# Kernel tuning notes

Measured on AMD Instinct MI355X. Metric: run time of the kernel, lower is better.

## Reference

```python
import jax, jax.numpy as jnp
import numpy as np


def _mlp(x, w1, b1, w2, b2):
    # generic 2-layer MLP (stand-in for ConfiguredModule's combine_mlp / embedding_mlp)
    return jax.nn.gelu(x @ w1 + b1) @ w2 + b2


def setup_inputs() -> dict:
    key = jax.random.key(0)
    ks = jax.random.split(key, 8)
    B, N, A = 8, 128, 64          # molecules, atoms, nfeature
    Rr, Ra = 32, 16               # radial / angular geometry shifts
    P = N * (N - 1) // 2          # 8128 atom pairs
    d_pair, H, nembed = 32, 512, 256

    def rnd(k, shp, scale=1.0):
        return jax.random.normal(k, shp, dtype=jnp.float32) * scale

    return {
        "gr": rnd(ks[0], (B, N, Rr, N), 0.1),
        "ga": rnd(ks[1], (B, N, Ra, P), 0.1),
        "afv": rnd(ks[2], (B, N, A)),
        # combine_mlp: 2A -> 2A -> d_pair
        "cw1": rnd(ks[3], (2 * A, 2 * A), 1.0 / np.sqrt(2 * A)),
        "cb1": jnp.zeros((2 * A,), jnp.float32),
        "cw2": rnd(ks[4], (2 * A, d_pair), 1.0 / np.sqrt(2 * A)),
        "cb2": jnp.zeros((d_pair,), jnp.float32),
        # embedding_mlp: Rr*A + Ra*d_pair -> H -> nembed
        "ew1": rnd(ks[5], (Rr * A + Ra * d_pair, H), 1.0 / np.sqrt(Rr * A + Ra * d_pair)),
        "eb1": jnp.zeros((H,), jnp.float32),
        "ew2": rnd(ks[6], (H, nembed), 1.0 / np.sqrt(H)),
        "eb2": jnp.zeros((nembed,), jnp.float32),
    }


def reference(gr, ga, afv, cw1, cb1, cw2, cb2, ew1, eb1, ew2, eb2):
    B, N, A = afv.shape
    # _combine_afv_1: pairwise outer sum/product, upper-triangular (i<j) pairs.
    # Instead of materializing [B, 2A, N, N] and masking, gather pairs directly
    # (row-major i<j order matches torch's triu boolean-mask indexing).
    ii, jj = jnp.triu_indices(N, k=1)           # [P]
    ai = afv[:, ii, :]                           # [B, P, A]
    aj = afv[:, jj, :]                           # [B, P, A]
    afv_pair = jnp.concatenate([ai + aj, ai * aj], axis=-1)  # [B, P, 2A]
    afv_pair = _mlp(afv_pair, cw1, cb1, cw2, cb2)            # [B, P, d_pair]

    # grv = matmul(gr, afv[:, None]) : [B, N, Rr, N] @ [B, 1, N, A] -> [B, N, Rr, A]
    grv = jnp.einsum('bnrm,bma->bnra', gr, afv).reshape(B, N, -1)
    # gav = matmul(ga, afv_pair[:, None]) : [B, N, Ra, P] @ [B, 1, P, d] -> [B, N, Ra, d]
    gav = jnp.einsum('bnap,bpd->bnad', ga, afv_pair).reshape(B, N, -1)

    aef = _mlp(jnp.concatenate([grv, gav], axis=-1), ew1, eb1, ew2, eb2)  # [B, N, nembed]
    return aef, afv
```

## Files before the change

kernel.cpp:

```cpp
#include <hip/hip_runtime.h>
#include <math.h>

#define BB 8
#define NN 128
#define AA 64
#define RR 32
#define RA 16
#define PP 8128
#define DP 32
#define HH 512
#define EE 256
#define XDIM 2560

static constexpr size_t WS_PAIRT = 0;
static constexpr size_t WS_XB    = WS_PAIRT + (size_t)BB*DP*PP/2;
static constexpr size_t WS_EW1B  = WS_XB + (size_t)BB*NN*XDIM/2;
static constexpr size_t WS_AFVT  = WS_EW1B + (size_t)HH*XDIM/2;
static constexpr size_t WS_CW1T  = WS_AFVT + (size_t)BB*AA*NN/2;
static constexpr size_t WS_CW2T  = WS_CW1T + (size_t)128*128/2;
static constexpr size_t WS_EW2B  = WS_CW2T + (size_t)DP*128/2;
static constexpr size_t WS_HB    = WS_EW2B + (size_t)EE*HH/2;

typedef __attribute__((ext_vector_type(8))) short bf16x8;
typedef __attribute__((ext_vector_type(4))) float f32x4;

__device__ __forceinline__ float gelu_f(float x) {
    float u = 0.7978845608028654f * (x + 0.044715f * x * x * x);
    float au = fabsf(u);
    float e = __expf(-2.0f * au);
    float th = (1.0f - e) / (1.0f + e);
    th = copysignf(th, u);
    return 0.5f * x * (1.0f + th);
}

__device__ __forceinline__ unsigned short f2bf(float x) {
    union { float f; unsigned u; } v; v.f = x;
    unsigned r = v.u + 0x7fffu + ((v.u >> 16) & 1u);
    return (unsigned short)(r >> 16);
}

__device__ __forceinline__ bf16x8 pack_bf16x8(float4 a, float4 b) {
    bf16x8 r;
    r[0] = (short)f2bf(a.x); r[1] = (short)f2bf(a.y);
    r[2] = (short)f2bf(a.z); r[3] = (short)f2bf(a.w);
    r[4] = (short)f2bf(b.x); r[5] = (short)f2bf(b.y);
    r[6] = (short)f2bf(b.z); r[7] = (short)f2bf(b.w);
    return r;
}

__global__ __launch_bounds__(256) void prep_k(
    const float* __restrict__ afv, const float* __restrict__ cw1,
    const float* __restrict__ cw2, unsigned short* __restrict__ afvT,
    unsigned short* __restrict__ cw1T, unsigned short* __restrict__ cw2T,
    float* __restrict__ out2)
{
    const int bid = blockIdx.x, t = threadIdx.x;
    if (bid < 64) {
        int idx = bid * 256 + t;
        int b = idx >> 11;
        int rem = idx & 2047;
        int a = rem >> 5;
        int m0 = (rem & 31) * 4;
        ushort4 o;
        o.x = f2bf(afv[((size_t)b * NN + m0 + 0) * AA + a]);
        o.y = f2bf(afv[((size_t)b * NN + m0 + 1) * AA + a]);
        o.z = f2bf(afv[((size_t)b * NN + m0 + 2) * AA + a]);
        o.w = f2bf(afv[((size_t)b * NN + m0 + 3) * AA + a]);
        *(ushort4*)(afvT + ((size_t)b * AA + a) * NN + m0) = o;
        float4 v = *(const float4*)(afv + (size_t)idx * 4);
        *(float4*)(out2 + (size_t)idx * 4) = v;
    } else if (bid < 80) {
        int idx = (bid - 64) * 256 + t;
        int n = idx >> 5;
        int k0 = (idx & 31) * 4;
        ushort4 o;
        o.x = f2bf(cw1[(size_t)(k0 + 0) * 128 + n]);
        o.y = f2bf(cw1[(size_t)(k0 + 1) * 128 + n]);
        o.z = f2bf(cw1[(size_t)(k0 + 2) * 128 + n]);
        o.w = f2bf(cw1[(size_t)(k0 + 3) * 128 + n]);
        *(ushort4*)(cw1T + (size_t)n * 128 + k0) = o;
    } else {
        int idx = (bid - 80) * 256 + t;
        int d = idx >> 5;
        int k0 = (idx & 31) * 4;
        ushort4 o;
        o.x = f2bf(cw2[(size_t)(k0 + 0) * DP + d]);
        o.y = f2bf(cw2[(size_t)(k0 + 1) * DP + d]);
        o.z = f2bf(cw2[(size_t)(k0 + 2) * DP + d]);
        o.w = f2bf(cw2[(size_t)(k0 + 3) * DP + d]);
        *(ushort4*)(cw2T + (size_t)d * 128 + k0) = o;
    }
}

#define NB_GRV 256
#define NB_PAIR 1016
#define NB_EW1 1280

__global__ __launch_bounds__(256) void stage1_k(
    const float* __restrict__ afv, const unsigned short* __restrict__ cw1T,
    const float* __restrict__ cb1, const unsigned short* __restrict__ cw2T,
    const float* __restrict__ cb2, unsigned short* __restrict__ pairT,
    const float* __restrict__ gr, unsigned short* __restrict__ Xb,
    const unsigned short* __restrict__ afvT,
    const float* __restrict__ ew1, unsigned short* __restrict__ ew1bT,
    const float* __restrict__ ew2, unsigned short* __restrict__ ew2bT)
{
    __shared__ unsigned short sm[16384];
    __shared__ int iis[64], jjs[64];
    const int bid = blockIdx.x;
    const int t = threadIdx.x;
    const int w = t >> 6, lane = t & 63;
    const int lm = lane & 15, lg = lane >> 4;

    if (bid >= NB_GRV + NB_PAIR + NB_EW1) {
        int q = (bid - (NB_GRV + NB_PAIR + NB_EW1)) * 256 + t;
        int n = q & 255;
        int k0 = (q >> 8) * 4;
        ushort4 o;
        o.x = f2bf(ew2[(size_t)(k0 + 0) * EE + n]);
        o.y = f2bf(ew2[(size_t)(k0 + 1) * EE + n]);
        o.z = f2bf(ew2[(size_t)(k0 + 2) * EE + n]);
        o.w = f2bf(ew2[(size_t)(k0 + 3) * EE + n]);
        *(ushort4*)(ew2bT + (size_t)n * HH + k0) = o;
        return;
    }
    if (bid >= NB_GRV + NB_PAIR) {
        int q = (bid - (NB_GRV + NB_PAIR)) * 256 + t;
        int n = q & 511;
        int k0 = (q >> 9) * 4;
        ushort4 o;
        o.x = f2bf(ew1[(size_t)(k0 + 0) * HH + n]);
        o.y = f2bf(ew1[(size_t)(k0 + 1) * HH + n]);
        o.z = f2bf(ew1[(size_t)(k0 + 2) * HH + n]);
        o.w = f2bf(ew1[(size_t)(k0 + 3) * HH + n]);
        *(ushort4*)(ew1bT + (size_t)n * XDIM + k0) = o;
        return;
    }

    if (bid < NB_GRV) {
        const int b = bid >> 5;
        const int rbase = (bid & 31) * 128;
        const float* gab = gr + ((size_t)b * 4096 + rbase) * NN;
        unsigned short* As = sm;
        const int srow = t >> 1, half = t & 1;
        const float* arow = gab + (size_t)srow * NN + half * 64;
        #pragma unroll
        for (int q = 0; q < 8; ++q) {
            float4 x0 = *(const float4*)(arow + q * 8);
            float4 x1 = *(const float4*)(arow + q * 8 + 4);
            bf16x8 v = pack_bf16x8(x0, x1);
            int g = half * 8 + q;
            *(bf16x8*)(As + srow * 128 + ((g ^ (srow & 7)) * 8)) = v;
        }
        __syncthreads();
        const int wm = w * 32;
        f32x4 acc[2][4];
        #pragma unroll
        for (int i = 0; i < 2; ++i)
            #pragma unroll
            for (int j = 0; j < 4; ++j) acc[i][j] = 0.f;
        const unsigned short* Bb = afvT + (size_t)b * AA * NN;
        #pragma unroll
        for (int ks = 0; ks < 4; ++ks) {
            int g = ks * 4 + lg;
            int r0 = wm + lm, r1 = wm + 16 + lm;
            bf16x8 a0 = *(const bf16x8*)(As + r0 * 128 + ((g ^ (r0 & 7)) * 8));
            bf16x8 a1 = *(const bf16x8*)(As + r1 * 128 + ((g ^ (r1 & 7)) * 8));
            #pragma unroll
            for (int ni = 0; ni < 4; ++ni) {
                bf16x8 bv = *(const bf16x8*)(Bb + (size_t)(ni * 16 + lm) * NN + ks * 32 + lg * 8);
                acc[0][ni] = __builtin_amdgcn_mfma_f32_16x16x32_bf16(a0, bv, acc[0][ni], 0, 0, 0);
                acc[1][ni] = __builtin_amdgcn_mfma_f32_16x16x32_bf16(a1, bv, acc[1][ni], 0, 0, 0);
            }
        }
        __syncthreads();
        unsigned short* T = sm;
        #pragma unroll
        for (int mi = 0; mi < 2; ++mi)
            #pragma unroll
            for (int ni = 0; ni < 4; ++ni)
                #pragma unroll
                for (int r = 0; r < 4; ++r)
                    T[(wm + mi * 16 + lg * 4 + r) * 64 + ni * 16 + lm] =
                        f2bf(acc[mi][ni][r]);
        __syncthreads();
        #pragma unroll
        for (int q = 0; q < 4; ++q) {
            int idx = t + q * 256;
            int rr2 = idx >> 3, slot = idx & 7;
            bf16x8 v = *(const bf16x8*)(T + rr2 * 64 + slot * 8);
            int grow = rbase + rr2;
            *(bf16x8*)(Xb + ((size_t)(b * NN) + (grow >> 5)) * XDIM +
                       (grow & 31) * 64 + slot * 8) = v;
        }
        return;
    }

    const int bid2 = bid - NB_GRV;
    const int b = bid2 / 127;
    const int pbase = (bid2 % 127) * 64;
    unsigned short* X = sm;
    unsigned short* Hs = sm + 8192;

    if (t < 64) {
        int p = pbase + t;
        int i = 0;
        while (i < 126) {
            int nx = i + 1;
            int off = nx * 127 - (nx * (nx - 1)) / 2;
            if (off <= p) i = nx; else break;
        }
        int off = i * 127 - (i * (i - 1)) / 2;
        iis[t] = i;
        jjs[t] = i + 1 + (p - off);
    }
    __syncthreads();
    {
        int pp = t & 63, seg = t >> 6;
        const float* ar = afv + (size_t)(b * NN + iis[pp]) * AA + seg * 16;
        const float* br = afv + (size_t)(b * NN + jjs[pp]) * AA + seg * 16;
        float4 xa = *(const float4*)(ar),     xb2 = *(const float4*)(ar + 4);
        float4 xc = *(const float4*)(ar + 8), xd = *(const float4*)(ar + 12);
        float4 ya = *(const float4*)(br),     yb = *(const float4*)(br + 4);
        float4 yc = *(const float4*)(br + 8), yd = *(const float4*)(br + 12);
        float4 s0 = make_float4(xa.x + ya.x, xa.y + ya.y, xa.z + ya.z, xa.w + ya.w);
        float4 s1 = make_float4(xb2.x + yb.x, xb2.y + yb.y, xb2.z + yb.z, xb2.w + yb.w);
        float4 s2 = make_float4(xc.x + yc.x, xc.y + yc.y, xc.z + yc.z, xc.w + yc.w);
        float4 s3 = make_float4(xd.x + yd.x, xd.y + yd.y, xd.z + yd.z, xd.w + yd.w);
        float4 p0 = make_float4(xa.x * ya.x, xa.y * ya.y, xa.z * ya.z, xa.w * ya.w);
        float4 p1 = make_float4(xb2.x * yb.x, xb2.y * yb.y, xb2.z * yb.z, xb2.w * yb.w);
        float4 p2 = make_float4(xc.x * yc.x, xc.y * yc.y, xc.z * yc.z, xc.w * yc.w);
        float4 p3 = make_float4(xd.x * yd.x, xd.y * yd.y, xd.z * yd.z, xd.w * yd.w);
        int gs = seg * 2, gp = 8 + seg * 2, sw = pp & 7;
        *(bf16x8*)(X + pp * 128 + (((gs + 0) ^ sw) * 8)) = pack_bf16x8(s0, s1);
        *(bf16x8*)(X + pp * 128 + (((gs + 1) ^ sw) * 8)) = pack_bf16x8(s2, s3);
        *(bf16x8*)(X + pp * 128 + (((gp + 0) ^ sw) * 8)) = pack_bf16x8(p0, p1);
        *(bf16x8*)(X + pp * 128 + (((gp + 1) ^ sw) * 8)) = pack_bf16x8(p2, p3);
    }
    __syncthreads();
    const int wn = w * 32;
    f32x4 acc1[4][2];
    #pragma unroll
    for (int i = 0; i < 4; ++i)
        #pragma unroll
        for (int j = 0; j < 2; ++j) acc1[i][j] = 0.f;
    #pragma unroll
    for (int ks = 0; ks < 4; ++ks) {
        int g = ks * 4 + lg;
        bf16x8 a[4];
        #pragma unroll
        for (int mi = 0; mi < 4; ++mi) {
            int row = mi * 16 + lm;
            a[mi] = *(const bf16x8*)(X + row * 128 + ((g ^ (row & 7)) * 8));
        }
        #pragma unroll
        for (int ni = 0; ni < 2; ++ni) {
            bf16x8 bv = *(const bf16x8*)(cw1T + (size_t)(wn + ni * 16 + lm) * 128 +
                                         ks * 32 + lg * 8);
            #pragma unroll
            for (int mi = 0; mi < 4; ++mi)
                acc1[mi][ni] = __builtin_amdgcn_mfma_f32_16x16x32_bf16(
                    a[mi], bv, acc1[mi][ni], 0, 0, 0);
        }
    }
    #pragma unroll
    for (int ni = 0; ni < 2; ++ni) {
        int n = wn + ni * 16 + lm;
        float bb = cb1[n];
        int gn = n >> 3, ne = n & 7;
        #pragma unroll
        for (int mi = 0; mi < 4; ++mi)
            #pragma unroll
            for (int r = 0; r < 4; ++r) {
                int row = mi * 16 + lg * 4 + r;
                Hs[row * 128 + ((gn ^ (row & 7)) * 8 + ne)] =
                    f2bf(gelu_f(acc1[mi][ni][r] + bb));
            }
    }
    __syncthreads();
    f32x4 acc2[2];
    acc2[0] = 0.f; acc2[1] = 0.f;
    #pragma unroll
    for (int ks = 0; ks < 4; ++ks) {
        int row = w * 16 + lm;
        int g = ks * 4 + lg;
        bf16x8 a2 = *(const bf16x8*)(Hs + row * 128 + ((g ^ (row & 7)) * 8));
        #pragma unroll
        for (int ni = 0; ni < 2; ++ni) {
            bf16x8 bv = *(const bf16x8*)(cw2T + (size_t)(ni * 16 + lm) * 128 +
                                         ks * 32 + lg * 8);
            acc2[ni] = __builtin_amdgcn_mfma_f32_16x16x32_bf16(a2, bv, acc2[ni], 0, 0, 0);
        }
    }
    {
        unsigned short* T = sm;
        #pragma unroll
        for (int ni = 0; ni < 2; ++ni) {
            int d = ni * 16 + lm;
            float bb = cb2[d];
            #pragma unroll
            for (int r = 0; r < 4; ++r) {
                int p = w * 16 + lg * 4 + r;
                T[d * 64 + p] = f2bf(acc2[ni][r] + bb);
            }
        }
        __syncthreads();
        int d = t >> 3, slot = t & 7;
        bf16x8 v = *(const bf16x8*)(T + d * 64 + slot * 8);
        *(bf16x8*)(pairT + ((size_t)b * DP + d) * PP + pbase + slot * 8) = v;
    }
}

__global__ __launch_bounds__(256) void gav_k(
    const float* __restrict__ ga, const unsigned short* __restrict__ pairT,
    unsigned short* __restrict__ Xb)
{
    __shared__ unsigned short As[32 * 64];
    __shared__ unsigned short Bs[32 * 64];
    const int bid = blockIdx.x;
    const int rt = bid & 63, b = bid >> 6;
    const int rbase = rt * 32;
    const int t = threadIdx.x;
    const int srow = t >> 3, slot = t & 7;
    const int w = t >> 6, lane = t & 63;
    const int lm = lane & 15, lg = lane >> 4;
    const int wr = (w & 1) * 16, wc = (w >> 1) * 16;

    f32x4 acc = 0.f;

    const float* gab = ga + (size_t)(b * 2048 + rbase) * PP;
    const unsigned short* pbT = pairT + (size_t)b * DP * PP;

    float4 ra0, ra1;
    bf16x8 rb;
    ra0 = *(const float4*)(gab + (size_t)srow * PP + slot * 8);
    ra1 = *(const float4*)(gab + (size_t)srow * PP + slot * 8 + 4);
    rb  = *(const bf16x8*)(pbT + (size_t)srow * PP + slot * 8);

    for (int it = 0; it < 127; ++it) {
        __syncthreads();
        int g = (slot ^ (srow & 7)) * 8;
        *(bf16x8*)(As + srow * 64 + g) = pack_bf16x8(ra0, ra1);
        *(bf16x8*)(Bs + srow * 64 + g) = rb;
        __syncthreads();
        if (it + 1 < 127) {
            int kn = (it + 1) * 64;
            ra0 = *(const float4*)(gab + (size_t)srow * PP + kn + slot * 8);
            ra1 = *(const float4*)(gab + (size_t)srow * PP + kn + slot * 8 + 4);
            rb  = *(const bf16x8*)(pbT + (size_t)srow * PP + kn + slot * 8);
        }
        #pragma unroll
        for (int ks = 0; ks < 2; ++ks) {
            int gg = ks * 4 + lg;
            int rowa = wr + lm;
            int rowb = wc + lm;
            bf16x8 a  = *(const bf16x8*)(As + rowa * 64 + ((gg ^ (rowa & 7)) * 8));
            bf16x8 bv = *(const bf16x8*)(Bs + rowb * 64 + ((gg ^ (rowb & 7)) * 8));
            acc = __builtin_amdgcn_mfma_f32_16x16x32_bf16(a, bv, acc, 0, 0, 0);
        }
    }
    #pragma unroll
    for (int r = 0; r < 4; ++r) {
        int grow = rbase + wr + lg * 4 + r;
        int n = grow >> 4, a2 = grow & 15;
        int d = wc + lm;
        Xb[(size_t)(b * NN + n) * XDIM + 2048 + a2 * DP + d] = f2bf(acc[r]);
    }
}

__global__ __launch_bounds__(256) void mlp1_k(
    const unsigned short* __restrict__ Xb,
    const unsigned short* __restrict__ Wt,
    const float* __restrict__ eb1, unsigned short* __restrict__ Hb)
{
    __shared__ unsigned short As[64 * 64];
    __shared__ unsigned short Bs[64 * 64];
    const int bid = blockIdx.x;
    const int ct = bid & 7, rt = bid >> 3;
    const int rbase = rt * 64, nbase = ct * 64;
    const int t = threadIdx.x;
    const int w = t >> 6, lane = t & 63;
    const int lm = lane & 15, lg = lane >> 4;
    const int srow = t >> 2, sg = (t & 3) * 2;

    f32x4 acc[4];
    #pragma unroll
    for (int i = 0; i < 4; ++i) acc[i] = 0.f;

    const unsigned short* Arow = Xb + (size_t)(rbase + srow) * XDIM;
    const unsigned short* Brow = Wt + (size_t)(nbase + srow) * XDIM;

    bf16x8 rA0, rA1, rB0, rB1;
    rA0 = *(const bf16x8*)(Arow + sg * 8);
    rA1 = *(const bf16x8*)(Arow + sg * 8 + 8);
    rB0 = *(const bf16x8*)(Brow + sg * 8);
    rB1 = *(const bf16x8*)(Brow + sg * 8 + 8);

    for (int it = 0; it < 40; ++it) {
        __syncthreads();
        int sw = srow & 7;
        *(bf16x8*)(As + srow * 64 + (((sg + 0) ^ sw) * 8)) = rA0;
        *(bf16x8*)(As + srow * 64 + (((sg + 1) ^ sw) * 8)) = rA1;
        *(bf16x8*)(Bs + srow * 64 + (((sg + 0) ^ sw) * 8)) = rB0;
        *(bf16x8*)(Bs + srow * 64 + (((sg + 1) ^ sw) * 8)) = rB1;
        __syncthreads();
        if (it + 1 < 40) {
            int kn = (it + 1) * 64;
            rA0 = *(const bf16x8*)(Arow + kn + sg * 8);
            rA1 = *(const bf16x8*)(Arow + kn + sg * 8 + 8);
            rB0 = *(const bf16x8*)(Brow + kn + sg * 8);
            rB1 = *(const bf16x8*)(Brow + kn + sg * 8 + 8);
        }
        #pragma unroll
        for (int ks = 0; ks < 2; ++ks) {
            int rowa = w * 16 + lm;
            int g = ks * 4 + lg;
            bf16x8 a = *(const bf16x8*)(As + rowa * 64 + ((g ^ (rowa & 7)) * 8));
            #pragma unroll
            for (int ni = 0; ni < 4; ++ni) {
                int rowb = ni * 16 + lm;
                bf16x8 bv = *(const bf16x8*)(Bs + rowb * 64 + ((g ^ (rowb & 7)) * 8));
                acc[ni] = __builtin_amdgcn_mfma_f32_16x16x32_bf16(a, bv, acc[ni], 0, 0, 0);
            }
        }
    }
    #pragma unroll
    for (int ni = 0; ni < 4; ++ni) {
        int col = nbase + ni * 16 + lm;
        float bb = eb1[col];
        #pragma unroll
        for (int r = 0; r < 4; ++r) {
            int row = rbase + w * 16 + lg * 4 + r;
            Hb[(size_t)row * HH + col] = f2bf(gelu_f(acc[ni][r] + bb));
        }
    }
}

__global__ __launch_bounds__(256) void mlp2_k(
    const unsigned short* __restrict__ Hb,
    const unsigned short* __restrict__ Wt,
    const float* __restrict__ eb2, float* __restrict__ out)
{
    __shared__ unsigned short As[64 * 64];
    __shared__ unsigned short Bs[64 * 64];
    const int bid = blockIdx.x;
    const int ct = bid & 3, rt = bid >> 2;
    const int rbase = rt * 64, nbase = ct * 64;
    const int t = threadIdx.x;
    const int w = t >> 6, lane = t & 63;
    const int lm = lane & 15, lg = lane >> 4;
    const int srow = t >> 2, sg = (t & 3) * 2;

    f32x4 acc[4];
    #pragma unroll
    for (int i = 0; i < 4; ++i) acc[i] = 0.f;

    const unsigned short* Arow = Hb + (size_t)(rbase + srow) * HH;
    const unsigned short* Brow = Wt + (size_t)(nbase + srow) * HH;

    bf16x8 rA0, rA1, rB0, rB1;
    rA0 = *(const bf16x8*)(Arow + sg * 8);
    rA1 = *(const bf16x8*)(Arow + sg * 8 + 8);
    rB0 = *(const bf16x8*)(Brow + sg * 8);
    rB1 = *(const bf16x8*)(Brow + sg * 8 + 8);

    for (int it = 0; it < 8; ++it) {
        __syncthreads();
        int sw = srow & 7;
        *(bf16x8*)(As + srow * 64 + (((sg + 0) ^ sw) * 8)) = rA0;
        *(bf16x8*)(As + srow * 64 + (((sg + 1) ^ sw) * 8)) = rA1;
        *(bf16x8*)(Bs + srow * 64 + (((sg + 0) ^ sw) * 8)) = rB0;
        *(bf16x8*)(Bs + srow * 64 + (((sg + 1) ^ sw) * 8)) = rB1;
        __syncthreads();
        if (it + 1 < 8) {
            int kn = (it + 1) * 64;
            rA0 = *(const bf16x8*)(Arow + kn + sg * 8);
            rA1 = *(const bf16x8*)(Arow + kn + sg * 8 + 8);
            rB0 = *(const bf16x8*)(Brow + kn + sg * 8);
            rB1 = *(const bf16x8*)(Brow + kn + sg * 8 + 8);
        }
        #pragma unroll
        for (int ks = 0; ks < 2; ++ks) {
            int rowa = w * 16 + lm;
            int g = ks * 4 + lg;
            bf16x8 a = *(const bf16x8*)(As + rowa * 64 + ((g ^ (rowa & 7)) * 8));
            #pragma unroll
            for (int ni = 0; ni < 4; ++ni) {
                int rowb = ni * 16 + lm;
                bf16x8 bv = *(const bf16x8*)(Bs + rowb * 64 + ((g ^ (rowb & 7)) * 8));
                acc[ni] = __builtin_amdgcn_mfma_f32_16x16x32_bf16(a, bv, acc[ni], 0, 0, 0);
            }
        }
    }
    #pragma unroll
    for (int ni = 0; ni < 4; ++ni) {
        int col = nbase + ni * 16 + lm;
        float bb = eb2[col];
        #pragma unroll
        for (int r = 0; r < 4; ++r) {
            int row = rbase + w * 16 + lg * 4 + r;
            out[(size_t)row * EE + col] = acc[ni][r] + bb;
        }
    }
}

extern "C" void kernel_launch(void* const* d_in, const int* in_sizes, int n_in,
                              void* d_out, int out_size, void* d_ws, size_t ws_size,
                              hipStream_t stream) {
    const float* gr  = (const float*)d_in[0];
    const float* ga  = (const float*)d_in[1];
    const float* afv = (const float*)d_in[2];
    const float* cw1 = (const float*)d_in[3];
    const float* cb1 = (const float*)d_in[4];
    const float* cw2 = (const float*)d_in[5];
    const float* cb2 = (const float*)d_in[6];
    const float* ew1 = (const float*)d_in[7];
    const float* eb1 = (const float*)d_in[8];
    const float* ew2 = (const float*)d_in[9];
    const float* eb2 = (const float*)d_in[10];
    float* out = (float*)d_out;
    float* ws = (float*)d_ws;

    unsigned short* pairT  = (unsigned short*)(ws + WS_PAIRT);
    unsigned short* Xb     = (unsigned short*)(ws + WS_XB);
    unsigned short* ew1bT  = (unsigned short*)(ws + WS_EW1B);
    unsigned short* afvT   = (unsigned short*)(ws + WS_AFVT);
    unsigned short* cw1T   = (unsigned short*)(ws + WS_CW1T);
    unsigned short* cw2T   = (unsigned short*)(ws + WS_CW2T);
    unsigned short* ew2bT  = (unsigned short*)(ws + WS_EW2B);
    unsigned short* Hb     = (unsigned short*)(ws + WS_HB);

    prep_k<<<dim3(84), dim3(256), 0, stream>>>(afv, cw1, cw2, afvT, cw1T, cw2T,
                                               out + (size_t)BB * NN * EE);
    stage1_k<<<dim3(2680), dim3(256), 0, stream>>>(afv, cw1T, cb1, cw2T, cb2, pairT,
                                                   gr, Xb, afvT, ew1, ew1bT,
                                                   ew2, ew2bT);
    gav_k<<<dim3(512), dim3(256), 0, stream>>>(ga, pairT, Xb);
    mlp1_k<<<dim3(128), dim3(256), 0, stream>>>(Xb, ew1bT, eb1, Hb);
    mlp2_k<<<dim3(64), dim3(256), 0, stream>>>(Hb, ew2bT, eb2, out);
}
```

Measured before the change: 201.3 us.

## Move weight conversion into gav kernel, double gav K-tile, halve MLP row tiles

The ew1/ew2 bf16 transpose blocks move from stage1 into the gav kernel launch, so they run alongside the memory-bound ga GEMM instead of lengthening stage1. The gav kernel now stages 128-wide K tiles, halving the loop trip count and barrier count, with a clamped tail load and a shortened final iteration. The MLP kernels use 32-row tiles so twice as many blocks launch and more CUs are filled. In exchange, each block gets less reuse and does more redundant loads of the weight tiles.

```diff
diff --git a/kernel.cpp b/kernel.cpp
--- a/kernel.cpp
+++ b/kernel.cpp
@@ -94,16 +94,13 @@
 
 #define NB_GRV 256
 #define NB_PAIR 1016
-#define NB_EW1 1280
 
 __global__ __launch_bounds__(256) void stage1_k(
     const float* __restrict__ afv, const unsigned short* __restrict__ cw1T,
     const float* __restrict__ cb1, const unsigned short* __restrict__ cw2T,
     const float* __restrict__ cb2, unsigned short* __restrict__ pairT,
     const float* __restrict__ gr, unsigned short* __restrict__ Xb,
-    const unsigned short* __restrict__ afvT,
-    const float* __restrict__ ew1, unsigned short* __restrict__ ew1bT,
-    const float* __restrict__ ew2, unsigned short* __restrict__ ew2bT)
+    const unsigned short* __restrict__ afvT)
 {
     __shared__ unsigned short sm[16384];
     __shared__ int iis[64], jjs[64];
@@ -111,31 +108,6 @@
     const int t = threadIdx.x;
     const int w = t >> 6, lane = t & 63;
     const int lm = lane & 15, lg = lane >> 4;
-
-    if (bid >= NB_GRV + NB_PAIR + NB_EW1) {
-        int q = (bid - (NB_GRV + NB_PAIR + NB_EW1)) * 256 + t;
-        int n = q & 255;
-        int k0 = (q >> 8) * 4;
-        ushort4 o;
-        o.x = f2bf(ew2[(size_t)(k0 + 0) * EE + n]);
-        o.y = f2bf(ew2[(size_t)(k0 + 1) * EE + n]);
-        o.z = f2bf(ew2[(size_t)(k0 + 2) * EE + n]);
-        o.w = f2bf(ew2[(size_t)(k0 + 3) * EE + n]);
-        *(ushort4*)(ew2bT + (size_t)n * HH + k0) = o;
-        return;
-    }
-    if (bid >= NB_GRV + NB_PAIR) {
-        int q = (bid - (NB_GRV + NB_PAIR)) * 256 + t;
-        int n = q & 511;
-        int k0 = (q >> 9) * 4;
-        ushort4 o;
-        o.x = f2bf(ew1[(size_t)(k0 + 0) * HH + n]);
-        o.y = f2bf(ew1[(size_t)(k0 + 1) * HH + n]);
-        o.z = f2bf(ew1[(size_t)(k0 + 2) * HH + n]);
-        o.w = f2bf(ew1[(size_t)(k0 + 3) * HH + n]);
-        *(ushort4*)(ew1bT + (size_t)n * XDIM + k0) = o;
-        return;
-    }
 
     if (bid < NB_GRV) {
         const int b = bid >> 5;
@@ -313,14 +285,42 @@
 
 __global__ __launch_bounds__(256) void gav_k(
     const float* __restrict__ ga, const unsigned short* __restrict__ pairT,
-    unsigned short* __restrict__ Xb)
+    unsigned short* __restrict__ Xb,
+    const float* __restrict__ ew1, unsigned short* __restrict__ ew1bT,
+    const float* __restrict__ ew2, unsigned short* __restrict__ ew2bT)
 {
-    __shared__ unsigned short As[32 * 64];
-    __shared__ unsigned short Bs[32 * 64];
+    __shared__ unsigned short As[32 * 128];
+    __shared__ unsigned short Bs[32 * 128];
     const int bid = blockIdx.x;
+    const int t = threadIdx.x;
+
+    if (bid >= 512 + 1280) {
+        int q = (bid - (512 + 1280)) * 256 + t;
+        int n = q & 255;
+        int k0 = (q >> 8) * 4;
+        ushort4 o;
+        o.x = f2bf(ew2[(size_t)(k0 + 0) * EE + n]);
+        o.y = f2bf(ew2[(size_t)(k0 + 1) * EE + n]);
+        o.z = f2bf(ew2[(size_t)(k0 + 2) * EE + n]);
+        o.w = f2bf(ew2[(size_t)(k0 + 3) * EE + n]);
+        *(ushort4*)(ew2bT + (size_t)n * HH + k0) = o;
+        return;
+    }
+    if (bid >= 512) {
+        int q = (bid - 512) * 256 + t;
+        int n = q & 511;
+        int k0 = (q >> 9) * 4;
+        ushort4 o;
+        o.x = f2bf(ew1[(size_t)(k0 + 0) * HH + n]);
+        o.y = f2bf(ew1[(size_t)(k0 + 1) * HH + n]);
+        o.z = f2bf(ew1[(size_t)(k0 + 2) * HH + n]);
+        o.w = f2bf(ew1[(size_t)(k0 + 3) * HH + n]);
+        *(ushort4*)(ew1bT + (size_t)n * XDIM + k0) = o;
+        return;
+    }
+
     const int rt = bid & 63, b = bid >> 6;
     const int rbase = rt * 32;
-    const int t = threadIdx.x;
     const int srow = t >> 3, slot = t & 7;
     const int w = t >> 6, lane = t & 63;
     const int lm = lane & 15, lg = lane >> 4;
@@ -331,32 +331,58 @@
     const float* gab = ga + (size_t)(b * 2048 + rbase) * PP;
     const unsigned short* pbT = pairT + (size_t)b * DP * PP;
 
-    float4 ra0, ra1;
-    bf16x8 rb;
-    ra0 = *(const float4*)(gab + (size_t)srow * PP + slot * 8);
-    ra1 = *(const float4*)(gab + (size_t)srow * PP + slot * 8 + 4);
-    rb  = *(const bf16x8*)(pbT + (size_t)srow * PP + slot * 8);
-
-    for (int it = 0; it < 127; ++it) {
-        __syncthreads();
-        int g = (slot ^ (srow & 7)) * 8;
-        *(bf16x8*)(As + srow * 64 + g) = pack_bf16x8(ra0, ra1);
-        *(bf16x8*)(Bs + srow * 64 + g) = rb;
-        __syncthreads();
-        if (it + 1 < 127) {
-            int kn = (it + 1) * 64;
-            ra0 = *(const float4*)(gab + (size_t)srow * PP + kn + slot * 8);
-            ra1 = *(const float4*)(gab + (size_t)srow * PP + kn + slot * 8 + 4);
-            rb  = *(const bf16x8*)(pbT + (size_t)srow * PP + kn + slot * 8);
-        }
-        #pragma unroll
-        for (int ks = 0; ks < 2; ++ks) {
-            int gg = ks * 4 + lg;
-            int rowa = wr + lm;
-            int rowb = wc + lm;
-            bf16x8 a  = *(const bf16x8*)(As + rowa * 64 + ((gg ^ (rowa & 7)) * 8));
-            bf16x8 bv = *(const bf16x8*)(Bs + rowb * 64 + ((gg ^ (rowb & 7)) * 8));
-            acc = __builtin_amdgcn_mfma_f32_16x16x32_bf16(a, bv, acc, 0, 0, 0);
+    float4 ra[4];
+    bf16x8 rb0, rb1;
+    {
+        int k0 = slot * 8;
+        ra[0] = *(const float4*)(gab + (size_t)srow * PP + k0);
+        ra[1] = *(const float4*)(gab + (size_t)srow * PP + k0 + 4);
+        ra[2] = *(const float4*)(gab + (size_t)srow * PP + k0 + 64);
+        ra[3] = *(const float4*)(gab + (size_t)srow * PP + k0 + 68);
+        rb0 = *(const bf16x8*)(pbT + (size_t)srow * PP + k0);
+        rb1 = *(const bf16x8*)(pbT + (size_t)srow * PP + k0 + 64);
+    }
+
+    for (int it = 0; it < 64; ++it) {
+        __syncthreads();
+        const int sw = srow & 7;
+        const int g0 = (slot ^ sw) * 8;
+        const int g1 = ((slot ^ sw) + 8) * 8;
+        *(bf16x8*)(As + srow * 128 + g0) = pack_bf16x8(ra[0], ra[1]);
+        *(bf16x8*)(As + srow * 128 + g1) = pack_bf16x8(ra[2], ra[3]);
+        *(bf16x8*)(Bs + srow * 128 + g0) = rb0;
+        *(bf16x8*)(Bs + srow * 128 + g1) = rb1;
+        __syncthreads();
+        if (it + 1 < 64) {
+            int kn = (it + 1) * 128 + slot * 8;
+            int k1 = kn + 64; if (k1 > PP - 8) k1 = PP - 8;
+            ra[0] = *(const float4*)(gab + (size_t)srow * PP + kn);
+            ra[1] = *(const float4*)(gab + (size_t)srow * PP + kn + 4);
+            ra[2] = *(const float4*)(gab + (size_t)srow * PP + k1);
+            ra[3] = *(const float4*)(gab + (size_t)srow * PP + k1 + 4);
+            rb0 = *(const bf16x8*)(pbT + (size_t)srow * PP + kn);
+            rb1 = *(const bf16x8*)(pbT + (size_t)srow * PP + k1);
+        }
+        if (it < 63) {
+            #pragma unroll
+            for (int ks = 0; ks < 4; ++ks) {
+                int gg = ks * 4 + lg;
+                int rowa = wr + lm;
+                int rowb = wc + lm;
+                bf16x8 a  = *(const bf16x8*)(As + rowa * 128 + ((gg ^ (rowa & 7)) * 8));
+                bf16x8 bv = *(const bf16x8*)(Bs + rowb * 128 + ((gg ^ (rowb & 7)) * 8));
+                acc = __builtin_amdgcn_mfma_f32_16x16x32_bf16(a, bv, acc, 0, 0, 0);
+            }
+        } else {
+            #pragma unroll
+            for (int ks = 0; ks < 2; ++ks) {
+                int gg = ks * 4 + lg;
+                int rowa = wr + lm;
+                int rowb = wc + lm;
+                bf16x8 a  = *(const bf16x8*)(As + rowa * 128 + ((gg ^ (rowa & 7)) * 8));
+                bf16x8 bv = *(const bf16x8*)(Bs + rowb * 128 + ((gg ^ (rowb & 7)) * 8));
+                acc = __builtin_amdgcn_mfma_f32_16x16x32_bf16(a, bv, acc, 0, 0, 0);
+            }
         }
     }
     #pragma unroll
@@ -373,67 +399,61 @@
     const unsigned short* __restrict__ Wt,
     const float* __restrict__ eb1, unsigned short* __restrict__ Hb)
 {
-    __shared__ unsigned short As[64 * 64];
+    __shared__ unsigned short As[32 * 64];
     __shared__ unsigned short Bs[64 * 64];
     const int bid = blockIdx.x;
     const int ct = bid & 7, rt = bid >> 3;
-    const int rbase = rt * 64, nbase = ct * 64;
+    const int rbase = rt * 32, nbase = ct * 64;
     const int t = threadIdx.x;
     const int w = t >> 6, lane = t & 63;
     const int lm = lane & 15, lg = lane >> 4;
-    const int srow = t >> 2, sg = (t & 3) * 2;
-
-    f32x4 acc[4];
-    #pragma unroll
-    for (int i = 0; i < 4; ++i) acc[i] = 0.f;
-
-    const unsigned short* Arow = Xb + (size_t)(rbase + srow) * XDIM;
-    const unsigned short* Brow = Wt + (size_t)(nbase + srow) * XDIM;
-
-    bf16x8 rA0, rA1, rB0, rB1;
-    rA0 = *(const bf16x8*)(Arow + sg * 8);
-    rA1 = *(const bf16x8*)(Arow + sg * 8 + 8);
-    rB0 = *(const bf16x8*)(Brow + sg * 8);
-    rB1 = *(const bf16x8*)(Brow + sg * 8 + 8);
+    const int srow = t >> 3, sg = t & 7;
+
+    f32x4 acc[2];
+    acc[0] = 0.f; acc[1] = 0.f;
+
+    const unsigned short* Arow  = Xb + (size_t)(rbase + srow) * XDIM;
+    const unsigned short* Brow0 = Wt + (size_t)(nbase + srow) * XDIM;
+    const unsigned short* Brow1 = Wt + (size_t)(nbase + srow + 32) * XDIM;
+
+    bf16x8 rA, rB0, rB1;
+    rA  = *(const bf16x8*)(Arow + sg * 8);
+    rB0 = *(const bf16x8*)(Brow0 + sg * 8);
+    rB1 = *(const bf16x8*)(Brow1 + sg * 8);
 
     for (int it = 0; it < 40; ++it) {
         __syncthreads();
-        int sw = srow & 7;
-        *(bf16x8*)(As + srow * 64 + (((sg + 0) ^ sw) * 8)) = rA0;
-        *(bf16x8*)(As + srow * 64 + (((sg + 1) ^ sw) * 8)) = rA1;
-        *(bf16x8*)(Bs + srow * 64 + (((sg + 0) ^ sw) * 8)) = rB0;
-        *(bf16x8*)(Bs + srow * 64 + (((sg + 1) ^ sw) * 8)) = rB1;
+        const int sw = srow & 7;
+        *(bf16x8*)(As + srow * 64 + ((sg ^ sw) * 8)) = rA;
+        *(bf16x8*)(Bs + srow * 64 + ((sg ^ sw) * 8)) = rB0;
+        *(bf16x8*)(Bs + (srow + 32) * 64 + ((sg ^ sw) * 8)) = rB1;
         __syncthreads();
         if (it + 1 < 40) {
             int kn = (it + 1) * 64;
-            rA0 = *(const bf16x8*)(Arow + kn + sg * 8);
-            rA1 = *(const bf16x8*)(Arow + kn + sg * 8 + 8);
-            rB0 = *(const bf16x8*)(Brow + kn + sg * 8);
-            rB1 = *(const bf16x8*)(Brow + kn + sg * 8 + 8);
+            rA  = *(const bf16x8*)(Arow + kn + sg * 8);
+            rB0 = *(const bf16x8*)(Brow0 + kn + sg * 8);
+            rB1 = *(const bf16x8*)(Brow1 + kn + sg * 8);
         }
         #pragma unroll
         for (int ks = 0; ks < 2; ++ks) {
-            int rowa = w * 16 + lm;
             int g = ks * 4 + lg;
-            bf16x8 a = *(const bf16x8*)(As + rowa * 64 + ((g ^ (rowa & 7)) * 8));
-            #pragma unroll
-            for (int ni = 0; ni < 4; ++ni) {
-                int rowb = ni * 16 + lm;
-                bf16x8 bv = *(const bf16x8*)(Bs + rowb * 64 + ((g ^ (rowb & 7)) * 8));
-                acc[ni] = __builtin_amdgcn_mfma_f32_16x16x32_bf16(a, bv, acc[ni], 0, 0, 0);
-            }
-        }
-    }
-    #pragma unroll
-    for (int ni = 0; ni < 4; ++ni) {
-        int col = nbase + ni * 16 + lm;
-        float bb = eb1[col];
+            int r0 = lm, r1 = 16 + lm, rb_ = w * 16 + lm;
+            bf16x8 a0 = *(const bf16x8*)(As + r0 * 64 + ((g ^ (r0 & 7)) * 8));
+            bf16x8 a1 = *(const bf16x8*)(As + r1 * 64 + ((g ^ (r1 & 7)) * 8));
+            bf16x8 bv = *(const bf16x8*)(Bs + rb_ * 64 + ((g ^ (rb_ & 7)) * 8));
+            acc[0] = __builtin_amdgcn_mfma_f32_16x16x32_bf16(a0, bv, acc[0], 0, 0, 0);
+            acc[1] = __builtin_amdgcn_mfma_f32_16x16x32_bf16(a1, bv, acc[1], 0, 0, 0);
+        }
+    }
+    const int col = nbase + w * 16 + lm;
+    const float bb = eb1[col];
+    #pragma unroll
+    for (int mi = 0; mi < 2; ++mi)
         #pragma unroll
         for (int r = 0; r < 4; ++r) {
-            int row = rbase + w * 16 + lg * 4 + r;
-            Hb[(size_t)row * HH + col] = f2bf(gelu_f(acc[ni][r] + bb));
-        }
-    }
+            int row = rbase + mi * 16 + lg * 4 + r;
+            Hb[(size_t)row * HH + col] = f2bf(gelu_f(acc[mi][r] + bb));
+        }
 }
 
 __global__ __launch_bounds__(256) void mlp2_k(
@@ -441,67 +461,61 @@
     const unsigned short* __restrict__ Wt,
     const float* __restrict__ eb2, float* __restrict__ out)
 {
-    __shared__ unsigned short As[64 * 64];
+    __shared__ unsigned short As[32 * 64];
     __shared__ unsigned short Bs[64 * 64];
     const int bid = blockIdx.x;
     const int ct = bid & 3, rt = bid >> 2;
-    const int rbase = rt * 64, nbase = ct * 64;
+    const int rbase = rt * 32, nbase = ct * 64;
     const int t = threadIdx.x;
     const int w = t >> 6, lane = t & 63;
     const int lm = lane & 15, lg = lane >> 4;
-    const int srow = t >> 2, sg = (t & 3) * 2;
-
-    f32x4 acc[4];
-    #pragma unroll
-    for (int i = 0; i < 4; ++i) acc[i] = 0.f;
-
-    const unsigned short* Arow = Hb + (size_t)(rbase + srow) * HH;
-    const unsigned short* Brow = Wt + (size_t)(nbase + srow) * HH;
-
-    bf16x8 rA0, rA1, rB0, rB1;
-    rA0 = *(const bf16x8*)(Arow + sg * 8);
-    rA1 = *(const bf16x8*)(Arow + sg * 8 + 8);
-    rB0 = *(const bf16x8*)(Brow + sg * 8);
-    rB1 = *(const bf16x8*)(Brow + sg * 8 + 8);
+    const int srow = t >> 3, sg = t & 7;
+
+    f32x4 acc[2];
+    acc[0] = 0.f; acc[1] = 0.f;
+
+    const unsigned short* Arow  = Hb + (size_t)(rbase + srow) * HH;
+    const unsigned short* Brow0 = Wt + (size_t)(nbase + srow) * HH;
+    const unsigned short* Brow1 = Wt + (size_t)(nbase + srow + 32) * HH;
+
+    bf16x8 rA, rB0, rB1;
+    rA  = *(const bf16x8*)(Arow + sg * 8);
+    rB0 = *(const bf16x8*)(Brow0 + sg * 8);
+    rB1 = *(const bf16x8*)(Brow1 + sg * 8);
 
     for (int it = 0; it < 8; ++it) {
         __syncthreads();
-        int sw = srow & 7;
-        *(bf16x8*)(As + srow * 64 + (((sg + 0) ^ sw) * 8)) = rA0;
-        *(bf16x8*)(As + srow * 64 + (((sg + 1) ^ sw) * 8)) = rA1;
-        *(bf16x8*)(Bs + srow * 64 + (((sg + 0) ^ sw) * 8)) = rB0;
-        *(bf16x8*)(Bs + srow * 64 + (((sg + 1) ^ sw) * 8)) = rB1;
+        const int sw = srow & 7;
+        *(bf16x8*)(As + srow * 64 + ((sg ^ sw) * 8)) = rA;
+        *(bf16x8*)(Bs + srow * 64 + ((sg ^ sw) * 8)) = rB0;
+        *(bf16x8*)(Bs + (srow + 32) * 64 + ((sg ^ sw) * 8)) = rB1;
         __syncthreads();
         if (it + 1 < 8) {
             int kn = (it + 1) * 64;
-            rA0 = *(const bf16x8*)(Arow + kn + sg * 8);
-            rA1 = *(const bf16x8*)(Arow + kn + sg * 8 + 8);
-            rB0 = *(const bf16x8*)(Brow + kn + sg * 8);
-            rB1 = *(const bf16x8*)(Brow + kn + sg * 8 + 8);
+            rA  = *(const bf16x8*)(Arow + kn + sg * 8);
+            rB0 = *(const bf16x8*)(Brow0 + kn + sg * 8);
+            rB1 = *(const bf16x8*)(Brow1 + kn + sg * 8);
         }
         #pragma unroll
         for (int ks = 0; ks < 2; ++ks) {
-            int rowa = w * 16 + lm;
             int g = ks * 4 + lg;
-            bf16x8 a = *(const bf16x8*)(As + rowa * 64 + ((g ^ (rowa & 7)) * 8));
-            #pragma unroll
-            for (int ni = 0; ni < 4; ++ni) {
-                int rowb = ni * 16 + lm;
-                bf16x8 bv = *(const bf16x8*)(Bs + rowb * 64 + ((g ^ (rowb & 7)) * 8));
-                acc[ni] = __builtin_amdgcn_mfma_f32_16x16x32_bf16(a, bv, acc[ni], 0, 0, 0);
-            }
-        }
-    }
-    #pragma unroll
-    for (int ni = 0; ni < 4; ++ni) {
-        int col = nbase + ni * 16 + lm;
-        float bb = eb2[col];
+            int r0 = lm, r1 = 16 + lm, rb_ = w * 16 + lm;
+            bf16x8 a0 = *(const bf16x8*)(As + r0 * 64 + ((g ^ (r0 & 7)) * 8));
+            bf16x8 a1 = *(const bf16x8*)(As + r1 * 64 + ((g ^ (r1 & 7)) * 8));
+            bf16x8 bv = *(const bf16x8*)(Bs + rb_ * 64 + ((g ^ (rb_ & 7)) * 8));
+            acc[0] = __builtin_amdgcn_mfma_f32_16x16x32_bf16(a0, bv, acc[0], 0, 0, 0);
+            acc[1] = __builtin_amdgcn_mfma_f32_16x16x32_bf16(a1, bv, acc[1], 0, 0, 0);
+        }
+    }
+    const int col = nbase + w * 16 + lm;
+    const float bb = eb2[col];
+    #pragma unroll
+    for (int mi = 0; mi < 2; ++mi)
         #pragma unroll
         for (int r = 0; r < 4; ++r) {
-            int row = rbase + w * 16 + lg * 4 + r;
-            out[(size_t)row * EE + col] = acc[ni][r] + bb;
-        }
-    }
+            int row = rbase + mi * 16 + lg * 4 + r;
+            out[(size_t)row * EE + col] = acc[mi][r] + bb;
+        }
 }
 
 extern "C" void kernel_launch(void* const* d_in, const int* in_sizes, int n_in,
@@ -532,10 +546,9 @@
 
     prep_k<<<dim3(84), dim3(256), 0, stream>>>(afv, cw1, cw2, afvT, cw1T, cw2T,
                                                out + (size_t)BB * NN * EE);
-    stage1_k<<<dim3(2680), dim3(256), 0, stream>>>(afv, cw1T, cb1, cw2T, cb2, pairT,
-                                                   gr, Xb, afvT, ew1, ew1bT,
-                                                   ew2, ew2bT);
-    gav_k<<<dim3(512), dim3(256), 0, stream>>>(ga, pairT, Xb);
-    mlp1_k<<<dim3(128), dim3(256), 0, stream>>>(Xb, ew1bT, eb1, Hb);
-    mlp2_k<<<dim3(64), dim3(256), 0, stream>>>(Hb, ew2bT, eb2, out);
-}
+    stage1_k<<<dim3(NB_GRV + NB_PAIR), dim3(256), 0, stream>>>(
+        afv, cw1T, cb1, cw2T, cb2, pairT, gr, Xb, afvT);
+    gav_k<<<dim3(1920), dim3(256), 0, stream>>>(ga, pairT, Xb, ew1, ew1bT, ew2, ew2bT);
+    mlp1_k<<<dim3(256), dim3(256), 0, stream>>>(Xb, ew1bT, eb1, Hb);
+    mlp2_k<<<dim3(128), dim3(256), 0, stream>>>(Hb, ew2bT, eb2, out);
+}
```

New measurement: 187.7 us. -6.7%, faster.
